# Kernel optimization log

Measured on AMD Instinct MI355X. Metric: run time of the kernel, lower is better.

The kernel has to match this reference:

```python
import jax, jax.numpy as jnp
from jax import lax
import numpy as np

N_BLOCKS = 5; C = 256; K = 1024; NQ = 8; NRES = 4; B = 2; T = 65536


def conv1d(x, w, b, stride=1, padding=0, dilation=1):
    # x: [N,C,T], w: [O,I,k]
    y = lax.conv_general_dilated(x, w, (stride,), [(padding, padding)],
                                 rhs_dilation=(dilation,),
                                 dimension_numbers=('NCH', 'OIH', 'NCH'))
    return y + b[None, :, None]


def conv_transpose1d(x, w, b):
    # PyTorch ConvTranspose1d(k=4, s=2, p=1); w: [in, out, 4]
    wk = jnp.swapaxes(jnp.flip(w, -1), 0, 1)  # [out, in, 4]
    y = lax.conv_general_dilated(x, wk, (1,), [(2, 2)], lhs_dilation=(2,),
                                 dimension_numbers=('NCH', 'OIH', 'NCH'))
    return y + b[None, :, None]


def residual_model(x, w0, b0, w1, b1, dil):
    # ReLU -> dilated conv3 -> ReLU -> conv3
    h = conv1d(jax.nn.relu(x), w0, b0, padding=dil, dilation=dil)
    h = conv1d(jax.nn.relu(h), w1, b1, padding=1)
    return h


def encoder(x, d0w, d0b, dw, db, rw, rb):
    for i in range(N_BLOCKS):
        if i == 0:
            x = conv1d(x, d0w, d0b, stride=2, padding=1)
        else:
            x = conv1d(x, dw[i - 1], db[i - 1], stride=2, padding=1)
        for j in range(NRES):
            dil = 3 ** (j + 1)
            # ResidualBlock.forward: x + model(x)
            x = x + residual_model(x, rw[i, j, 0], rb[i, j, 0], rw[i, j, 1], rb[i, j, 1], dil)
    return x


def decoder(x, rw, rb, uw, ub, ulw, ulb):
    for i in range(N_BLOCKS):
        for j in range(NRES):
            dil = 3 ** (j + 1)
            # DecoderBlock: x = x + ResidualBlock(x) = x + (x + model(x))
            x = x + (x + residual_model(x, rw[i, j, 0], rb[i, j, 0], rw[i, j, 1], rb[i, j, 1], dil))
        if i == N_BLOCKS - 1:
            x = conv_transpose1d(x, ulw, ulb)
        else:
            x = conv_transpose1d(x, uw[i], ub[i])
    return x


def rvq(emb, rvq_sum, rvq_usage):
    # emb: [N, C]; eval-mode residual VQ (no EMA update)
    q = jnp.zeros_like(emb)
    commit = jnp.asarray(0.0, emb.dtype)
    codes = []
    for i in range(NQ):
        cb = rvq_sum[i] / jnp.clip(rvq_usage[i], 1e-5, None)[:, None]  # [K, C]
        res = emb - q
        # argmin of squared distance over codebook rows (||res||^2 constant per column)
        scores = jnp.sum(cb * cb, axis=1)[:, None] - 2.0 * (cb @ res.T)  # [K, N]
        c = jnp.argmin(scores, axis=0)
        eq = cb[c]  # [N, C]
        eq_st = res + lax.stop_gradient(eq - res)  # straight-through
        commit = commit + jnp.mean((lax.stop_gradient(eq_st) - res) ** 2)
        q = q + eq_st
        codes.append(c.astype(jnp.int32))
    return jnp.stack(codes, axis=1), q, commit


def setup_inputs() -> dict:
    key = jax.random.key(0)
    ks = iter(jax.random.split(key, 16))

    def W(shape, fan_in):
        return (jax.random.normal(next(ks), shape, jnp.float32) / np.float32(np.sqrt(fan_in)))

    return {
        'x': jax.random.normal(next(ks), (B, 1, T), jnp.float32),
        'enc_down0_w': W((C, 1, 4), 4),
        'enc_down0_b': jnp.zeros((C,), jnp.float32),
        'enc_down_w': W((N_BLOCKS - 1, C, C, 4), C * 4),
        'enc_down_b': jnp.zeros((N_BLOCKS - 1, C), jnp.float32),
        'enc_res_w': W((N_BLOCKS, NRES, 2, C, C, 3), C * 3),
        'enc_res_b': jnp.zeros((N_BLOCKS, NRES, 2, C), jnp.float32),
        'dec_res_w': W((N_BLOCKS, NRES, 2, C, C, 3), C * 3),
        'dec_res_b': jnp.zeros((N_BLOCKS, NRES, 2, C), jnp.float32),
        'dec_up_w': W((N_BLOCKS - 1, C, C, 4), C * 4),
        'dec_up_b': jnp.zeros((N_BLOCKS - 1, C), jnp.float32),
        'dec_up_last_w': W((C, 1, 4), C * 4),
        'dec_up_last_b': jnp.zeros((1,), jnp.float32),
        'rvq_sum': jax.random.normal(next(ks), (NQ, K, C), jnp.float32) * 0.1,
        'rvq_usage': jnp.ones((NQ, K), jnp.float32),
    }


def reference(x, enc_down0_w, enc_down0_b, enc_down_w, enc_down_b, enc_res_w, enc_res_b,
              dec_res_w, dec_res_b, dec_up_w, dec_up_b, dec_up_last_w, dec_up_last_b,
              rvq_sum, rvq_usage):
    z = encoder(x, enc_down0_w, enc_down0_b, enc_down_w, enc_down_b, enc_res_w, enc_res_b)
    Bz, Cz, Tz = z.shape
    emb = jnp.transpose(z, (0, 2, 1)).reshape(Bz * Tz, Cz)  # (b t) c
    codes, q, commit = rvq(emb, rvq_sum, rvq_usage)
    zq = jnp.transpose(q.reshape(Bz, Tz, Cz), (0, 2, 1))  # b c t
    recon = decoder(zq, dec_res_w, dec_res_b, dec_up_w, dec_up_b, dec_up_last_w, dec_up_last_b)
    return recon, codes, commit
```

## Files before the change

kernel.cpp:

```cpp
#include <hip/hip_runtime.h>
#include <cstdint>

#define DEVFN static __device__ __forceinline__
typedef unsigned short ushort_t;
typedef unsigned int uint_t;
typedef short short8 __attribute__((ext_vector_type(8)));
typedef float f32x4 __attribute__((ext_vector_type(4)));

DEVFN float bf2f(ushort_t h) { return __uint_as_float(((uint_t)h) << 16); }
DEVFN ushort_t bfhi(float f) {
    uint_t u = __float_as_uint(f);
    u += 0x7fffu + ((u >> 16) & 1u);
    return (ushort_t)(u >> 16);
}
DEVFN void fsplit(float f, ushort_t& h, ushort_t& l) {
    h = bfhi(f);
    l = bfhi(f - bf2f(h));
}
DEVFN void relu_pair(uint_t& h, uint_t& l) {
    float f0 = bf2f((ushort_t)(h & 0xffffu)) + bf2f((ushort_t)(l & 0xffffu));
    float f1 = bf2f((ushort_t)(h >> 16)) + bf2f((ushort_t)(l >> 16));
    if (f0 <= 0.f) { h &= 0xffff0000u; l &= 0xffff0000u; }
    if (f1 <= 0.f) { h &= 0x0000ffffu; l &= 0x0000ffffu; }
}

__global__ __launch_bounds__(256)
void wprep3_k(const float* __restrict__ erw, const float* __restrict__ drw,
              ushort_t* __restrict__ wH, ushort_t* __restrict__ wL)
{
    const int gid = blockIdx.x * 256 + threadIdx.x;
    const int conv = gid >> 16;
    const int rem  = gid & 65535;
    const int co = rem >> 8, ci = rem & 255;
    const float* src = (conv < 40) ? (erw + (size_t)conv * 196608)
                                   : (drw + (size_t)(conv - 40) * 196608);
    const float* p = src + ((size_t)co * 256 + ci) * 3;
    ushort_t* oh = wH + (size_t)conv * 196608 + rem;
    ushort_t* ol = wL + (size_t)conv * 196608 + rem;
#pragma unroll
    for (int k = 0; k < 3; ++k) {
        ushort_t h, l; fsplit(p[k], h, l);
        oh[k * 65536] = h; ol[k * 65536] = l;
    }
}

__global__ __launch_bounds__(256)
void wprep4_k(const float* __restrict__ edw, const float* __restrict__ duw,
              ushort_t* __restrict__ wH, ushort_t* __restrict__ wL)
{
    const int gid = blockIdx.x * 256 + threadIdx.x;
    const int conv = gid >> 16;
    const int rem  = gid & 65535;
    const int co = rem >> 8, ci = rem & 255;
    ushort_t* oh = wH + (size_t)conv * 262144 + rem;
    ushort_t* ol = wL + (size_t)conv * 262144 + rem;
#pragma unroll
    for (int k = 0; k < 4; ++k) {
        float f;
        if (conv < 4)  f = edw[(size_t)conv * 262144 + ((size_t)co * 256 + ci) * 4 + k];
        else           f = duw[(size_t)(conv - 4) * 262144 + ((size_t)ci * 256 + co) * 4 + k];
        ushort_t h, l; fsplit(f, h, l);
        oh[k * 65536] = h; ol[k * 65536] = l;
    }
}

template<int TAPS, int STRIDE, bool RELU, int NT, int DMAX>
__global__ __launch_bounds__(256, (NT >= 8) ? 2 : 3)
void convs_k(const ushort_t* __restrict__ inH, const ushort_t* __restrict__ inL,
             const ushort_t* __restrict__ wH, const ushort_t* __restrict__ wL,
             const float* __restrict__ bias,
             const ushort_t* __restrict__ srcH, const ushort_t* __restrict__ srcL,
             float alpha,
             ushort_t* __restrict__ outH, ushort_t* __restrict__ outL,
             int Lin, int Lout, int dil, int pad)
{
    constexpr int ROWS = NT * 16;
    constexpr int SMAX = STRIDE * (ROWS - 1) + (TAPS - 1) * DMAX + 1;
    constexpr int XSB  = SMAX * 40 * 2;
    constexpr int ARENA = (2 * XSB > 16640) ? 2 * XSB : 16640;
    __shared__ __align__(16) char sarena[ARENA];
    ushort_t (*xsH)[40] = (ushort_t(*)[40])(sarena);
    ushort_t (*xsL)[40] = (ushort_t(*)[40])(sarena + XSB);

    const int tid = threadIdx.x;
    const int b = blockIdx.z;
    const int t0 = blockIdx.x * ROWS;
    const int wave = tid >> 6, lane = tid & 63;
    const int quad = lane >> 4, lr = lane & 15;
    const int cow = wave * 64;
    const size_t inbase = (size_t)b * Lin * 256;
    const int S = STRIDE * (ROWS - 1) + (TAPS - 1) * dil + 1;
    const int g0 = STRIDE * t0 - pad;

    f32x4 acc[4][NT];
#pragma unroll
    for (int m = 0; m < 4; ++m)
#pragma unroll
        for (int n = 0; n < NT; ++n) acc[m][n] = (f32x4)0.f;

    for (int chunk = 0; chunk < 8; ++chunk) {
        const int ci0 = chunk * 32;
        __syncthreads();
        for (int idx = tid; idx < S * 4; idx += 256) {
            const int s = idx >> 2, p = idx & 3;
            const int t = g0 + s;
            uint4 hv = make_uint4(0, 0, 0, 0), lv = hv;
            if (t >= 0 && t < Lin) {
                const size_t g = inbase + (size_t)t * 256 + ci0 + p * 8;
                hv = *(const uint4*)(inH + g);
                lv = *(const uint4*)(inL + g);
                if (RELU) {
                    relu_pair(hv.x, lv.x); relu_pair(hv.y, lv.y);
                    relu_pair(hv.z, lv.z); relu_pair(hv.w, lv.w);
                }
            }
            *(uint4*)&xsH[s][p * 8] = hv;
            *(uint4*)&xsL[s][p * 8] = lv;
        }
        __syncthreads();
#pragma unroll
        for (int tap = 0; tap < TAPS; ++tap) {
            const ushort_t* wHt = wH + (size_t)tap * 65536 + ci0 + quad * 8;
            const ushort_t* wLt = wL + (size_t)tap * 65536 + ci0 + quad * 8;
            short8 aH[4], aL[4];
#pragma unroll
            for (int m = 0; m < 4; ++m) {
                const int co = cow + m * 16 + lr;
                aH[m] = *(const short8*)(wHt + co * 256);
                aL[m] = *(const short8*)(wLt + co * 256);
            }
            const int rb = tap * dil;
#pragma unroll
            for (int n = 0; n < NT; ++n) {
                const int srow = STRIDE * (n * 16 + lr) + rb;
                const short8 bH = *(const short8*)&xsH[srow][quad * 8];
                const short8 bL = *(const short8*)&xsL[srow][quad * 8];
#pragma unroll
                for (int m = 0; m < 4; ++m)
                    acc[m][n] = __builtin_amdgcn_mfma_f32_16x16x32_bf16(aH[m], bH, acc[m][n], 0, 0, 0);
#pragma unroll
                for (int m = 0; m < 4; ++m)
                    acc[m][n] = __builtin_amdgcn_mfma_f32_16x16x32_bf16(aH[m], bL, acc[m][n], 0, 0, 0);
#pragma unroll
                for (int m = 0; m < 4; ++m)
                    acc[m][n] = __builtin_amdgcn_mfma_f32_16x16x32_bf16(aL[m], bH, acc[m][n], 0, 0, 0);
            }
        }
    }
    float4 bvv[4];
#pragma unroll
    for (int m = 0; m < 4; ++m)
        bvv[m] = *(const float4*)&bias[cow + m * 16 + quad * 4];
    __syncthreads();
    float (*ebuf)[260] = (float(*)[260])sarena;
#pragma unroll
    for (int n = 0; n < NT; ++n) {
#pragma unroll
        for (int m = 0; m < 4; ++m) {
            float4 v;
            v.x = acc[m][n][0] + bvv[m].x;
            v.y = acc[m][n][1] + bvv[m].y;
            v.z = acc[m][n][2] + bvv[m].z;
            v.w = acc[m][n][3] + bvv[m].w;
            *(float4*)&ebuf[lr][cow + m * 16 + quad * 4] = v;
        }
        __syncthreads();
        {
            const int row = tid >> 4;
            const int c00 = (tid & 15) * 4;
            const int t = t0 + n * 16 + row;
            const size_t gr = ((size_t)b * Lout + t) * 256;
#pragma unroll
            for (int rep = 0; rep < 4; ++rep) {
                const int col = c00 + rep * 64;
                float4 v = *(const float4*)&ebuf[row][col];
                if (alpha != 0.f) {
                    const ushort4 sh = *(const ushort4*)(srcH + gr + col);
                    const ushort4 sl = *(const ushort4*)(srcL + gr + col);
                    v.x += alpha * (bf2f(sh.x) + bf2f(sl.x));
                    v.y += alpha * (bf2f(sh.y) + bf2f(sl.y));
                    v.z += alpha * (bf2f(sh.z) + bf2f(sl.z));
                    v.w += alpha * (bf2f(sh.w) + bf2f(sl.w));
                }
                ushort4 oh, ol;
                fsplit(v.x, oh.x, ol.x); fsplit(v.y, oh.y, ol.y);
                fsplit(v.z, oh.z, ol.z); fsplit(v.w, oh.w, ol.w);
                *(ushort4*)(outH + gr + col) = oh;
                *(ushort4*)(outL + gr + col) = ol;
            }
        }
        __syncthreads();
    }
}

template<int NTc>
__global__ __launch_bounds__(256, 2)
void convt_k(const ushort_t* __restrict__ inH, const ushort_t* __restrict__ inL,
             const ushort_t* __restrict__ wH, const ushort_t* __restrict__ wL,
             const float* __restrict__ bias,
             ushort_t* __restrict__ outH, ushort_t* __restrict__ outL, int Lin)
{
    constexpr int ROWS = NTc * 16;
    constexpr int S = ROWS + 2;
    constexpr int XSB = S * 40 * 2;
    constexpr int ARENA = (2 * XSB > 33280) ? 2 * XSB : 33280;
    __shared__ __align__(16) char sarena[ARENA];
    ushort_t (*xsH)[40] = (ushort_t(*)[40])(sarena);
    ushort_t (*xsL)[40] = (ushort_t(*)[40])(sarena + XSB);

    const int tid = threadIdx.x;
    const int b = blockIdx.z;
    const int m0 = blockIdx.x * ROWS;
    const int Lout = Lin * 2;
    const int wave = tid >> 6, lane = tid & 63;
    const int quad = lane >> 4, lr = lane & 15;
    const int cow = wave * 64;
    const size_t inbase = (size_t)b * Lin * 256;

    f32x4 acc[4][NTc][2];
#pragma unroll
    for (int m = 0; m < 4; ++m)
#pragma unroll
        for (int n = 0; n < NTc; ++n) { acc[m][n][0] = (f32x4)0.f; acc[m][n][1] = (f32x4)0.f; }

    for (int chunk = 0; chunk < 8; ++chunk) {
        const int ci0 = chunk * 32;
        __syncthreads();
        for (int idx = tid; idx < S * 4; idx += 256) {
            const int s = idx >> 2, p = idx & 3;
            const int t = m0 - 1 + s;
            uint4 hv = make_uint4(0, 0, 0, 0), lv = hv;
            if (t >= 0 && t < Lin) {
                const size_t g = inbase + (size_t)t * 256 + ci0 + p * 8;
                hv = *(const uint4*)(inH + g);
                lv = *(const uint4*)(inL + g);
            }
            *(uint4*)&xsH[s][p * 8] = hv;
            *(uint4*)&xsL[s][p * 8] = lv;
        }
        __syncthreads();
#pragma unroll
        for (int tap = 0; tap < 4; ++tap) {
            const int ph = (tap == 0 || tap == 2) ? 1 : 0;
            const int sh = (tap == 0) ? 1 : ((tap == 3) ? -1 : 0);
            const ushort_t* wHt = wH + (size_t)tap * 65536 + ci0 + quad * 8;
            const ushort_t* wLt = wL + (size_t)tap * 65536 + ci0 + quad * 8;
            short8 aH[4], aL[4];
#pragma unroll
            for (int m = 0; m < 4; ++m) {
                const int co = cow + m * 16 + lr;
                aH[m] = *(const short8*)(wHt + co * 256);
                aL[m] = *(const short8*)(wLt + co * 256);
            }
#pragma unroll
            for (int n = 0; n < NTc; ++n) {
                const int srow = n * 16 + lr + sh + 1;
                const short8 bH = *(const short8*)&xsH[srow][quad * 8];
                const short8 bL = *(const short8*)&xsL[srow][quad * 8];
#pragma unroll
                for (int m = 0; m < 4; ++m)
                    acc[m][n][ph] = __builtin_amdgcn_mfma_f32_16x16x32_bf16(aH[m], bH, acc[m][n][ph], 0, 0, 0);
#pragma unroll
                for (int m = 0; m < 4; ++m)
                    acc[m][n][ph] = __builtin_amdgcn_mfma_f32_16x16x32_bf16(aH[m], bL, acc[m][n][ph], 0, 0, 0);
#pragma unroll
                for (int m = 0; m < 4; ++m)
                    acc[m][n][ph] = __builtin_amdgcn_mfma_f32_16x16x32_bf16(aL[m], bH, acc[m][n][ph], 0, 0, 0);
            }
        }
    }
    float4 bvv[4];
#pragma unroll
    for (int m = 0; m < 4; ++m)
        bvv[m] = *(const float4*)&bias[cow + m * 16 + quad * 4];
    __syncthreads();
    float (*ebuf)[260] = (float(*)[260])sarena;
#pragma unroll
    for (int n = 0; n < NTc; ++n) {
#pragma unroll
        for (int m = 0; m < 4; ++m) {
#pragma unroll
            for (int ph = 0; ph < 2; ++ph) {
                float4 v;
                v.x = acc[m][n][ph][0] + bvv[m].x;
                v.y = acc[m][n][ph][1] + bvv[m].y;
                v.z = acc[m][n][ph][2] + bvv[m].z;
                v.w = acc[m][n][ph][3] + bvv[m].w;
                *(float4*)&ebuf[2 * lr + ph][cow + m * 16 + quad * 4] = v;
            }
        }
        __syncthreads();
        {
            const int baset = 2 * (m0 + n * 16);
#pragma unroll
            for (int h = 0; h < 8; ++h) {
                const int row = (tid >> 4) + 16 * (h >> 2);
                const int col = (tid & 15) * 4 + (h & 3) * 64;
                const int t = baset + row;
                const size_t gr = ((size_t)b * Lout + t) * 256 + col;
                float4 v = *(const float4*)&ebuf[row][col];
                ushort4 oh, ol;
                fsplit(v.x, oh.x, ol.x); fsplit(v.y, oh.y, ol.y);
                fsplit(v.z, oh.z, ol.z); fsplit(v.w, oh.w, ol.w);
                *(ushort4*)(outH + gr) = oh;
                *(ushort4*)(outL + gr) = ol;
            }
        }
        __syncthreads();
    }
}

__global__ __launch_bounds__(256)
void down0_k2(const float* __restrict__ x, const float* __restrict__ w,
              const float* __restrict__ bias,
              ushort_t* __restrict__ outH, ushort_t* __restrict__ outL)
{
    const int t = blockIdx.x;
    const int b = blockIdx.y;
    const int co = threadIdx.x;
    const float* xb = x + (size_t)b * 65536;
    const float4 wv = *(const float4*)(w + co * 4);
    float s = bias[co];
    const int ti0 = 2 * t - 1;
    if (ti0 >= 0)      s = fmaf(xb[ti0], wv.x, s);
    s = fmaf(xb[ti0 + 1], wv.y, s);
    s = fmaf(xb[ti0 + 2], wv.z, s);
    if (ti0 + 3 < 65536) s = fmaf(xb[ti0 + 3], wv.w, s);
    ushort_t h, l; fsplit(s, h, l);
    const size_t g = ((size_t)b * 32768 + t) * 256 + co;
    outH[g] = h; outL[g] = l;
}

__global__ __launch_bounds__(256)
void uplast_k2(const ushort_t* __restrict__ inH, const ushort_t* __restrict__ inL,
               const float* __restrict__ w, const float* __restrict__ bias,
               float* __restrict__ out, int Lin)
{
    const int m = blockIdx.x * 256 + threadIdx.x;
    const int b = blockIdx.y;
    const float bv = bias[0];
    float aE = bv, aO = bv;
    const size_t base = (size_t)b * Lin * 256;
    const ushort_t* r0H = inH + base + (size_t)m * 256;
    const ushort_t* r0L = inL + base + (size_t)m * 256;
    const bool hasM = (m > 0), hasP = (m + 1 < Lin);
    for (int c0 = 0; c0 < 256; c0 += 8) {
        uint4 h0 = *(const uint4*)(r0H + c0);
        uint4 l0 = *(const uint4*)(r0L + c0);
        uint4 hm = make_uint4(0,0,0,0), lm = hm, hp = hm, lp = hm;
        if (hasM) { hm = *(const uint4*)(r0H - 256 + c0); lm = *(const uint4*)(r0L - 256 + c0); }
        if (hasP) { hp = *(const uint4*)(r0H + 256 + c0); lp = *(const uint4*)(r0L + 256 + c0); }
        const uint_t* h0p = (const uint_t*)&h0; const uint_t* l0p = (const uint_t*)&l0;
        const uint_t* hmp = (const uint_t*)&hm; const uint_t* lmp = (const uint_t*)&lm;
        const uint_t* hpp = (const uint_t*)&hp; const uint_t* lpp = (const uint_t*)&lp;
#pragma unroll
        for (int e = 0; e < 4; ++e) {
#pragma unroll
            for (int half = 0; half < 2; ++half) {
                const int sh = half * 16;
                const int ci = c0 + e * 2 + half;
                const float x0  = bf2f((ushort_t)(h0p[e] >> sh)) + bf2f((ushort_t)(l0p[e] >> sh));
                const float xm1 = bf2f((ushort_t)(hmp[e] >> sh)) + bf2f((ushort_t)(lmp[e] >> sh));
                const float xp1 = bf2f((ushort_t)(hpp[e] >> sh)) + bf2f((ushort_t)(lpp[e] >> sh));
                const float4 wv = *(const float4*)(w + ci * 4);
                aE = fmaf(x0, wv.y, fmaf(xm1, wv.w, aE));
                aO = fmaf(xp1, wv.x, fmaf(x0, wv.z, aO));
            }
        }
    }
    *(float2*)(out + (size_t)b * 2 * Lin + 2 * m) = make_float2(aE, aO);
}

__global__ void emb_k(const ushort_t* __restrict__ H, const ushort_t* __restrict__ L,
                      float* __restrict__ emb)
{
    const size_t g = (size_t)blockIdx.x * 256 + threadIdx.x;
    emb[g] = bf2f(H[g]) + bf2f(L[g]);
}
__global__ void qsplit_k(const float* __restrict__ q,
                         ushort_t* __restrict__ H, ushort_t* __restrict__ L)
{
    const size_t g = (size_t)blockIdx.x * 256 + threadIdx.x;
    ushort_t h, l; fsplit(q[g], h, l);
    H[g] = h; L[g] = l;
}

__global__ __launch_bounds__(256)
void rvq_cb_k(const float* __restrict__ sum, const float* __restrict__ usage,
              float* __restrict__ cb, float* __restrict__ cbT,
              float* __restrict__ cbn, int iq)
{
    const int k = blockIdx.x, c = threadIdx.x;
    const float den = fmaxf(usage[iq * 1024 + k], 1e-5f);
    const float v = sum[((size_t)iq * 1024 + k) * 256 + c] / den;
    cb[(size_t)k * 256 + c] = v;
    cbT[(size_t)c * 1024 + k] = v;
    float s = v * v;
    for (int off = 32; off; off >>= 1) s += __shfl_down(s, off, 64);
    __shared__ float ls[4];
    if ((c & 63) == 0) ls[c >> 6] = s;
    __syncthreads();
    if (c == 0) cbn[k] = ls[0] + ls[1] + ls[2] + ls[3];
}

DEVFN unsigned int ordbits(float f)
{
    unsigned u = __float_as_uint(f);
    return (u & 0x80000000u) ? ~u : (u | 0x80000000u);
}
DEVFN unsigned long long shfl_xor_u64(unsigned long long v, int mask)
{
    int lo = (int)(v & 0xffffffffull), hi = (int)(v >> 32);
    lo = __shfl_xor(lo, mask, 64);
    hi = __shfl_xor(hi, mask, 64);
    return ((unsigned long long)(unsigned)hi << 32) | (unsigned)lo;
}

__global__ __launch_bounds__(256)
void rvq_argmin_k(const float* __restrict__ emb, const float* __restrict__ q,
                  const float* __restrict__ cbT, const float* __restrict__ cbn,
                  int* __restrict__ codes, float* __restrict__ codes_out, int iq)
{
    const int n0 = blockIdx.x * 16;
    const int tid = threadIdx.x;
    __shared__ float res[16][256];
    for (int idx = tid; idx < 16 * 256; idx += 256) {
        int nl = idx >> 8, c = idx & 255;
        size_t g = (size_t)(n0 + nl) * 256 + c;
        res[nl][c] = emb[g] - q[g];
    }
    __syncthreads();
    float dot[16][4];
#pragma unroll
    for (int nl = 0; nl < 16; ++nl)
#pragma unroll
        for (int j = 0; j < 4; ++j) dot[nl][j] = 0.f;

    const float* cbtp = cbT + tid * 4;
    for (int c = 0; c < 256; ++c) {
        const float4 cbv = *(const float4*)(cbtp + (size_t)c * 1024);
#pragma unroll
        for (int nl = 0; nl < 16; ++nl) {
            const float r = res[nl][c];
            dot[nl][0] = fmaf(cbv.x, r, dot[nl][0]);
            dot[nl][1] = fmaf(cbv.y, r, dot[nl][1]);
            dot[nl][2] = fmaf(cbv.z, r, dot[nl][2]);
            dot[nl][3] = fmaf(cbv.w, r, dot[nl][3]);
        }
    }
    const float4 nrm = *(const float4*)(cbn + tid * 4);
    __shared__ unsigned long long wred[4][16];
    const int wave = tid >> 6, lane = tid & 63;
#pragma unroll
    for (int nl = 0; nl < 16; ++nl) {
        float s0 = nrm.x - 2.f * dot[nl][0];
        float s1 = nrm.y - 2.f * dot[nl][1];
        float s2 = nrm.z - 2.f * dot[nl][2];
        float s3 = nrm.w - 2.f * dot[nl][3];
        unsigned long long key =
            ((unsigned long long)ordbits(s0) << 32) | (unsigned)(tid * 4 + 0);
        unsigned long long k1 =
            ((unsigned long long)ordbits(s1) << 32) | (unsigned)(tid * 4 + 1);
        unsigned long long k2 =
            ((unsigned long long)ordbits(s2) << 32) | (unsigned)(tid * 4 + 2);
        unsigned long long k3 =
            ((unsigned long long)ordbits(s3) << 32) | (unsigned)(tid * 4 + 3);
        if (k1 < key) key = k1;
        if (k2 < key) key = k2;
        if (k3 < key) key = k3;
        for (int off = 32; off; off >>= 1) {
            unsigned long long o = shfl_xor_u64(key, off);
            if (o < key) key = o;
        }
        if (lane == 0) wred[wave][nl] = key;
    }
    __syncthreads();
    if (tid < 16) {
        unsigned long long bkey = wred[0][tid];
        if (wred[1][tid] < bkey) bkey = wred[1][tid];
        if (wred[2][tid] < bkey) bkey = wred[2][tid];
        if (wred[3][tid] < bkey) bkey = wred[3][tid];
        const int code = (int)(bkey & 0xffffffffull);
        codes[(size_t)(n0 + tid) * 8 + iq] = code;
        codes_out[(size_t)(n0 + tid) * 8 + iq] = (float)code;
    }
}

__global__ __launch_bounds__(256)
void rvq_update_k(const float* __restrict__ emb, float* __restrict__ q,
                  const float* __restrict__ cb, const int* __restrict__ codes,
                  float* __restrict__ commit, int iq)
{
    const int n = blockIdx.x, c = threadIdx.x;
    const int code = codes[(size_t)n * 8 + iq];
    const size_t g = (size_t)n * 256 + c;
    const float qv = q[g] + cb[(size_t)code * 256 + c];
    q[g] = qv;
    const float e = qv - emb[g];
    float s = e * e;
    for (int off = 32; off; off >>= 1) s += __shfl_down(s, off, 64);
    __shared__ float ls[4];
    if ((c & 63) == 0) ls[c >> 6] = s;
    __syncthreads();
    if (c == 0) atomicAdd(commit, ls[0] + ls[1] + ls[2] + ls[3]);
}

__global__ void commit_write_k(const float* __restrict__ commit, float* __restrict__ out)
{
    out[0] = commit[0] * (1.f / (4096.f * 256.f));
}

extern "C" void kernel_launch(void* const* d_in, const int* in_sizes, int n_in,
                              void* d_out, int out_size, void* d_ws, size_t ws_size,
                              hipStream_t stream)
{
    const float* x    = (const float*)d_in[0];
    const float* ed0w = (const float*)d_in[1];
    const float* ed0b = (const float*)d_in[2];
    const float* edw  = (const float*)d_in[3];
    const float* edb  = (const float*)d_in[4];
    const float* erw  = (const float*)d_in[5];
    const float* erb  = (const float*)d_in[6];
    const float* drw  = (const float*)d_in[7];
    const float* drb  = (const float*)d_in[8];
    const float* duw  = (const float*)d_in[9];
    const float* dub  = (const float*)d_in[10];
    const float* dulw = (const float*)d_in[11];
    const float* dulb = (const float*)d_in[12];
    const float* rsum = (const float*)d_in[13];
    const float* rusg = (const float*)d_in[14];
    float* out = (float*)d_out;

    char* base = (char*)d_ws;
    size_t o = 0;
    ushort_t* wH3 = (ushort_t*)(base + o); o += 31457280;
    ushort_t* wL3 = (ushort_t*)(base + o); o += 31457280;
    ushort_t* w4H = (ushort_t*)(base + o); o += 4194304;
    ushort_t* w4L = (ushort_t*)(base + o); o += 4194304;
    ushort_t* AH  = (ushort_t*)(base + o); o += 33554432;
    ushort_t* AL  = (ushort_t*)(base + o); o += 33554432;
    ushort_t* BH  = (ushort_t*)(base + o); o += 33554432;
    ushort_t* BL  = (ushort_t*)(base + o); o += 33554432;
    float* emb    = (float*)(base + o);    o += 4194304;
    float* q      = (float*)(base + o);    o += 4194304;
    float* commit = (float*)(base + o);    o += 64;
    float* cb     = (float*)(base + o);    o += 1048576;
    float* cbT    = (float*)(base + o);    o += 1048576;
    float* cbn    = (float*)(base + o);    o += 4096;
    int*   codes  = (int*)(base + o);      o += 131072;

    static const int DIL[4] = {3, 9, 27, 81};

    hipMemsetAsync(q, 0, 4194304 + 64, stream);

    wprep3_k<<<20480, 256, 0, stream>>>(erw, drw, wH3, wL3);
    wprep4_k<<<2048, 256, 0, stream>>>(edw, duw, w4H, w4L);

    auto conv3 = [&](const ushort_t* iH, const ushort_t* iL,
                     const ushort_t* wh, const ushort_t* wl, const float* bb,
                     const ushort_t* sH, const ushort_t* sL, float alpha,
                     ushort_t* oH, ushort_t* oL, int L, int d) {
        if (L >= 16384)
            convs_k<3, 1, true, 8, 81><<<dim3(L / 128, 1, 2), 256, 0, stream>>>(
                iH, iL, wh, wl, bb, sH, sL, alpha, oH, oL, L, L, d, d);
        else if (L >= 8192)
            convs_k<3, 1, true, 4, 81><<<dim3(L / 64, 1, 2), 256, 0, stream>>>(
                iH, iL, wh, wl, bb, sH, sL, alpha, oH, oL, L, L, d, d);
        else if (L >= 4096)
            convs_k<3, 1, true, 2, 81><<<dim3(L / 32, 1, 2), 256, 0, stream>>>(
                iH, iL, wh, wl, bb, sH, sL, alpha, oH, oL, L, L, d, d);
        else
            convs_k<3, 1, true, 1, 81><<<dim3(L / 16, 1, 2), 256, 0, stream>>>(
                iH, iL, wh, wl, bb, sH, sL, alpha, oH, oL, L, L, d, d);
    };

    down0_k2<<<dim3(32768, 2), 256, 0, stream>>>(x, ed0w, ed0b, AH, AL);
    int L = 32768;
    for (int i = 0; i < 5; ++i) {
        if (i > 0) {
            const ushort_t* wh = w4H + (size_t)(i - 1) * 262144;
            const ushort_t* wl = w4L + (size_t)(i - 1) * 262144;
            const int Lout = L / 2;
            if (Lout >= 16384)
                convs_k<4, 2, false, 8, 1><<<dim3(Lout / 128, 1, 2), 256, 0, stream>>>(
                    AH, AL, wh, wl, edb + (i - 1) * 256, AH, AL, 0.f, BH, BL, L, Lout, 1, 1);
            else if (Lout >= 8192)
                convs_k<4, 2, false, 4, 1><<<dim3(Lout / 64, 1, 2), 256, 0, stream>>>(
                    AH, AL, wh, wl, edb + (i - 1) * 256, AH, AL, 0.f, BH, BL, L, Lout, 1, 1);
            else if (Lout >= 4096)
                convs_k<4, 2, false, 2, 1><<<dim3(Lout / 32, 1, 2), 256, 0, stream>>>(
                    AH, AL, wh, wl, edb + (i - 1) * 256, AH, AL, 0.f, BH, BL, L, Lout, 1, 1);
            else
                convs_k<4, 2, false, 1, 1><<<dim3(Lout / 16, 1, 2), 256, 0, stream>>>(
                    AH, AL, wh, wl, edb + (i - 1) * 256, AH, AL, 0.f, BH, BL, L, Lout, 1, 1);
            ushort_t* t;
            t = AH; AH = BH; BH = t;
            t = AL; AL = BL; BL = t;
            L = Lout;
        }
        for (int j = 0; j < 4; ++j) {
            const int d = DIL[j];
            const size_t u = (size_t)(i * 4 + j) * 2;
            conv3(AH, AL, wH3 + (u + 0) * 196608, wL3 + (u + 0) * 196608,
                  erb + (u + 0) * 256, AH, AL, 0.f, BH, BL, L, d);
            conv3(BH, BL, wH3 + (u + 1) * 196608, wL3 + (u + 1) * 196608,
                  erb + (u + 1) * 256, AH, AL, 1.f, AH, AL, L, 1);
        }
    }

    emb_k<<<4096, 256, 0, stream>>>(AH, AL, emb);
    for (int iq = 0; iq < 8; ++iq) {
        rvq_cb_k<<<1024, 256, 0, stream>>>(rsum, rusg, cb, cbT, cbn, iq);
        rvq_argmin_k<<<256, 256, 0, stream>>>(emb, q, cbT, cbn, codes, out + 131072, iq);
        rvq_update_k<<<4096, 256, 0, stream>>>(emb, q, cb, codes, commit, iq);
    }
    qsplit_k<<<4096, 256, 0, stream>>>(q, AH, AL);

    L = 2048;
    for (int i = 0; i < 5; ++i) {
        for (int j = 0; j < 4; ++j) {
            const int d = DIL[j];
            const size_t u = 40 + (size_t)(i * 4 + j) * 2;
            conv3(AH, AL, wH3 + (u + 0) * 196608, wL3 + (u + 0) * 196608,
                  drb + ((size_t)(i * 4 + j) * 2 + 0) * 256, AH, AL, 0.f, BH, BL, L, d);
            conv3(BH, BL, wH3 + (u + 1) * 196608, wL3 + (u + 1) * 196608,
                  drb + ((size_t)(i * 4 + j) * 2 + 1) * 256, AH, AL, 2.f, AH, AL, L, 1);
        }
        if (i < 4) {
            const ushort_t* wh = w4H + (size_t)(4 + i) * 262144;
            const ushort_t* wl = w4L + (size_t)(4 + i) * 262144;
            if (L >= 16384)
                convt_k<4><<<dim3(L / 64, 1, 2), 256, 0, stream>>>(
                    AH, AL, wh, wl, dub + i * 256, BH, BL, L);
            else if (L >= 8192)
                convt_k<4><<<dim3(L / 64, 1, 2), 256, 0, stream>>>(
                    AH, AL, wh, wl, dub + i * 256, BH, BL, L);
            else if (L >= 4096)
                convt_k<2><<<dim3(L / 32, 1, 2), 256, 0, stream>>>(
                    AH, AL, wh, wl, dub + i * 256, BH, BL, L);
            else
                convt_k<1><<<dim3(L / 16, 1, 2), 256, 0, stream>>>(
                    AH, AL, wh, wl, dub + i * 256, BH, BL, L);
            ushort_t* t;
            t = AH; AH = BH; BH = t;
            t = AL; AL = BL; BL = t;
            L *= 2;
        } else {
            uplast_k2<<<dim3(L / 256, 2), 256, 0, stream>>>(AH, AL, dulw, dulb, out, L);
        }
    }

    commit_write_k<<<1, 1, 0, stream>>>(commit, out + 163840);
}
```

Baseline: 6.102 ms.

## Split conv3 output channels across blocks and specialize strided downsample kernel

```diff
diff --git a/kernel.cpp b/kernel.cpp
--- a/kernel.cpp
+++ b/kernel.cpp
@@ -64,39 +64,41 @@
     }
 }
 
-template<int TAPS, int STRIDE, bool RELU, int NT, int DMAX>
-__global__ __launch_bounds__(256, (NT >= 8) ? 2 : 3)
-void convs_k(const ushort_t* __restrict__ inH, const ushort_t* __restrict__ inL,
-             const ushort_t* __restrict__ wH, const ushort_t* __restrict__ wL,
-             const float* __restrict__ bias,
-             const ushort_t* __restrict__ srcH, const ushort_t* __restrict__ srcL,
-             float alpha,
-             ushort_t* __restrict__ outH, ushort_t* __restrict__ outL,
-             int Lin, int Lout, int dil, int pad)
-{
-    constexpr int ROWS = NT * 16;
-    constexpr int SMAX = STRIDE * (ROWS - 1) + (TAPS - 1) * DMAX + 1;
+template<bool RELU, int NTT>
+__global__ __launch_bounds__(256, 4)
+void conv3n_k(const ushort_t* __restrict__ inH, const ushort_t* __restrict__ inL,
+              const ushort_t* __restrict__ wH, const ushort_t* __restrict__ wL,
+              const float* __restrict__ bias,
+              const ushort_t* __restrict__ srcH, const ushort_t* __restrict__ srcL,
+              float alpha,
+              ushort_t* __restrict__ outH, ushort_t* __restrict__ outL,
+              int L, int dil)
+{
+    constexpr int ROWS = NTT * 16;
+    constexpr int SMAX = ROWS + 162;
     constexpr int XSB  = SMAX * 40 * 2;
-    constexpr int ARENA = (2 * XSB > 16640) ? 2 * XSB : 16640;
+    constexpr int EBUF = 16 * 132 * 4;
+    constexpr int ARENA = (2 * XSB > EBUF) ? 2 * XSB : EBUF;
     __shared__ __align__(16) char sarena[ARENA];
     ushort_t (*xsH)[40] = (ushort_t(*)[40])(sarena);
     ushort_t (*xsL)[40] = (ushort_t(*)[40])(sarena + XSB);
 
     const int tid = threadIdx.x;
     const int b = blockIdx.z;
+    const int co0 = blockIdx.y * 128;
     const int t0 = blockIdx.x * ROWS;
     const int wave = tid >> 6, lane = tid & 63;
     const int quad = lane >> 4, lr = lane & 15;
-    const int cow = wave * 64;
-    const size_t inbase = (size_t)b * Lin * 256;
-    const int S = STRIDE * (ROWS - 1) + (TAPS - 1) * dil + 1;
-    const int g0 = STRIDE * t0 - pad;
-
-    f32x4 acc[4][NT];
-#pragma unroll
-    for (int m = 0; m < 4; ++m)
-#pragma unroll
-        for (int n = 0; n < NT; ++n) acc[m][n] = (f32x4)0.f;
+    const int cow = co0 + wave * 32;
+    const size_t inbase = (size_t)b * L * 256;
+    const int S = ROWS + 2 * dil;
+    const int g0 = t0 - dil;
+
+    f32x4 acc[2][NTT];
+#pragma unroll
+    for (int m = 0; m < 2; ++m)
+#pragma unroll
+        for (int n = 0; n < NTT; ++n) acc[m][n] = (f32x4)0.f;
 
     for (int chunk = 0; chunk < 8; ++chunk) {
         const int ci0 = chunk * 32;
@@ -105,7 +107,7 @@
             const int s = idx >> 2, p = idx & 3;
             const int t = g0 + s;
             uint4 hv = make_uint4(0, 0, 0, 0), lv = hv;
-            if (t >= 0 && t < Lin) {
+            if (t >= 0 && t < L) {
                 const size_t g = inbase + (size_t)t * 256 + ci0 + p * 8;
                 hv = *(const uint4*)(inH + g);
                 lv = *(const uint4*)(inL + g);
@@ -119,59 +121,59 @@
         }
         __syncthreads();
 #pragma unroll
-        for (int tap = 0; tap < TAPS; ++tap) {
+        for (int tap = 0; tap < 3; ++tap) {
             const ushort_t* wHt = wH + (size_t)tap * 65536 + ci0 + quad * 8;
             const ushort_t* wLt = wL + (size_t)tap * 65536 + ci0 + quad * 8;
-            short8 aH[4], aL[4];
-#pragma unroll
-            for (int m = 0; m < 4; ++m) {
+            short8 aH[2], aL[2];
+#pragma unroll
+            for (int m = 0; m < 2; ++m) {
                 const int co = cow + m * 16 + lr;
                 aH[m] = *(const short8*)(wHt + co * 256);
                 aL[m] = *(const short8*)(wLt + co * 256);
             }
             const int rb = tap * dil;
 #pragma unroll
-            for (int n = 0; n < NT; ++n) {
-                const int srow = STRIDE * (n * 16 + lr) + rb;
+            for (int n = 0; n < NTT; ++n) {
+                const int srow = n * 16 + lr + rb;
                 const short8 bH = *(const short8*)&xsH[srow][quad * 8];
                 const short8 bL = *(const short8*)&xsL[srow][quad * 8];
 #pragma unroll
-                for (int m = 0; m < 4; ++m)
+                for (int m = 0; m < 2; ++m)
                     acc[m][n] = __builtin_amdgcn_mfma_f32_16x16x32_bf16(aH[m], bH, acc[m][n], 0, 0, 0);
 #pragma unroll
-                for (int m = 0; m < 4; ++m)
+                for (int m = 0; m < 2; ++m)
                     acc[m][n] = __builtin_amdgcn_mfma_f32_16x16x32_bf16(aH[m], bL, acc[m][n], 0, 0, 0);
 #pragma unroll
-                for (int m = 0; m < 4; ++m)
+                for (int m = 0; m < 2; ++m)
                     acc[m][n] = __builtin_amdgcn_mfma_f32_16x16x32_bf16(aL[m], bH, acc[m][n], 0, 0, 0);
             }
         }
     }
-    float4 bvv[4];
-#pragma unroll
-    for (int m = 0; m < 4; ++m)
+    float4 bvv[2];
+#pragma unroll
+    for (int m = 0; m < 2; ++m)
         bvv[m] = *(const float4*)&bias[cow + m * 16 + quad * 4];
     __syncthreads();
-    float (*ebuf)[260] = (float(*)[260])sarena;
-#pragma unroll
-    for (int n = 0; n < NT; ++n) {
-#pragma unroll
-        for (int m = 0; m < 4; ++m) {
+    float (*ebuf)[132] = (float(*)[132])sarena;
+#pragma unroll
+    for (int n = 0; n < NTT; ++n) {
+#pragma unroll
+        for (int m = 0; m < 2; ++m) {
             float4 v;
             v.x = acc[m][n][0] + bvv[m].x;
             v.y = acc[m][n][1] + bvv[m].y;
             v.z = acc[m][n][2] + bvv[m].z;
             v.w = acc[m][n][3] + bvv[m].w;
-            *(float4*)&ebuf[lr][cow + m * 16 + quad * 4] = v;
+            *(float4*)&ebuf[lr][wave * 32 + m * 16 + quad * 4] = v;
         }
         __syncthreads();
         {
             const int row = tid >> 4;
             const int c00 = (tid & 15) * 4;
             const int t = t0 + n * 16 + row;
-            const size_t gr = ((size_t)b * Lout + t) * 256;
-#pragma unroll
-            for (int rep = 0; rep < 4; ++rep) {
+            const size_t gr = ((size_t)b * L + t) * 256 + co0;
+#pragma unroll
+            for (int rep = 0; rep < 2; ++rep) {
                 const int col = c00 + rep * 64;
                 float4 v = *(const float4*)&ebuf[row][col];
                 if (alpha != 0.f) {
@@ -182,6 +184,120 @@
                     v.z += alpha * (bf2f(sh.z) + bf2f(sl.z));
                     v.w += alpha * (bf2f(sh.w) + bf2f(sl.w));
                 }
+                ushort4 oh, ol;
+                fsplit(v.x, oh.x, ol.x); fsplit(v.y, oh.y, ol.y);
+                fsplit(v.z, oh.z, ol.z); fsplit(v.w, oh.w, ol.w);
+                *(ushort4*)(outH + gr + col) = oh;
+                *(ushort4*)(outL + gr + col) = ol;
+            }
+        }
+        __syncthreads();
+    }
+}
+
+template<int NT>
+__global__ __launch_bounds__(256, (NT >= 8) ? 2 : 3)
+void convs_k(const ushort_t* __restrict__ inH, const ushort_t* __restrict__ inL,
+             const ushort_t* __restrict__ wH, const ushort_t* __restrict__ wL,
+             const float* __restrict__ bias,
+             ushort_t* __restrict__ outH, ushort_t* __restrict__ outL,
+             int Lin, int Lout)
+{
+    constexpr int ROWS = NT * 16;
+    constexpr int SMAX = 2 * (ROWS - 1) + 4;
+    constexpr int XSB  = SMAX * 40 * 2;
+    constexpr int ARENA = (2 * XSB > 16640) ? 2 * XSB : 16640;
+    __shared__ __align__(16) char sarena[ARENA];
+    ushort_t (*xsH)[40] = (ushort_t(*)[40])(sarena);
+    ushort_t (*xsL)[40] = (ushort_t(*)[40])(sarena + XSB);
+
+    const int tid = threadIdx.x;
+    const int b = blockIdx.z;
+    const int t0 = blockIdx.x * ROWS;
+    const int wave = tid >> 6, lane = tid & 63;
+    const int quad = lane >> 4, lr = lane & 15;
+    const int cow = wave * 64;
+    const size_t inbase = (size_t)b * Lin * 256;
+    const int S = 2 * (ROWS - 1) + 4;
+    const int g0 = 2 * t0 - 1;
+
+    f32x4 acc[4][NT];
+#pragma unroll
+    for (int m = 0; m < 4; ++m)
+#pragma unroll
+        for (int n = 0; n < NT; ++n) acc[m][n] = (f32x4)0.f;
+
+    for (int chunk = 0; chunk < 8; ++chunk) {
+        const int ci0 = chunk * 32;
+        __syncthreads();
+        for (int idx = tid; idx < S * 4; idx += 256) {
+            const int s = idx >> 2, p = idx & 3;
+            const int t = g0 + s;
+            uint4 hv = make_uint4(0, 0, 0, 0), lv = hv;
+            if (t >= 0 && t < Lin) {
+                const size_t g = inbase + (size_t)t * 256 + ci0 + p * 8;
+                hv = *(const uint4*)(inH + g);
+                lv = *(const uint4*)(inL + g);
+            }
+            *(uint4*)&xsH[s][p * 8] = hv;
+            *(uint4*)&xsL[s][p * 8] = lv;
+        }
+        __syncthreads();
+#pragma unroll
+        for (int tap = 0; tap < 4; ++tap) {
+            const ushort_t* wHt = wH + (size_t)tap * 65536 + ci0 + quad * 8;
+            const ushort_t* wLt = wL + (size_t)tap * 65536 + ci0 + quad * 8;
+            short8 aH[4], aL[4];
+#pragma unroll
+            for (int m = 0; m < 4; ++m) {
+                const int co = cow + m * 16 + lr;
+                aH[m] = *(const short8*)(wHt + co * 256);
+                aL[m] = *(const short8*)(wLt + co * 256);
+            }
+#pragma unroll
+            for (int n = 0; n < NT; ++n) {
+                const int srow = 2 * (n * 16 + lr) + tap;
+                const short8 bH = *(const short8*)&xsH[srow][quad * 8];
+                const short8 bL = *(const short8*)&xsL[srow][quad * 8];
+#pragma unroll
+                for (int m = 0; m < 4; ++m)
+                    acc[m][n] = __builtin_amdgcn_mfma_f32_16x16x32_bf16(aH[m], bH, acc[m][n], 0, 0, 0);
+#pragma unroll
+                for (int m = 0; m < 4; ++m)
+                    acc[m][n] = __builtin_amdgcn_mfma_f32_16x16x32_bf16(aH[m], bL, acc[m][n], 0, 0, 0);
+#pragma unroll
+                for (int m = 0; m < 4; ++m)
+                    acc[m][n] = __builtin_amdgcn_mfma_f32_16x16x32_bf16(aL[m], bH, acc[m][n], 0, 0, 0);
+            }
+        }
+    }
+    float4 bvv[4];
+#pragma unroll
+    for (int m = 0; m < 4; ++m)
+        bvv[m] = *(const float4*)&bias[cow + m * 16 + quad * 4];
+    __syncthreads();
+    float (*ebuf)[260] = (float(*)[260])sarena;
+#pragma unroll
+    for (int n = 0; n < NT; ++n) {
+#pragma unroll
+        for (int m = 0; m < 4; ++m) {
+            float4 v;
+            v.x = acc[m][n][0] + bvv[m].x;
+            v.y = acc[m][n][1] + bvv[m].y;
+            v.z = acc[m][n][2] + bvv[m].z;
+            v.w = acc[m][n][3] + bvv[m].w;
+            *(float4*)&ebuf[lr][cow + m * 16 + quad * 4] = v;
+        }
+        __syncthreads();
+        {
+            const int row = tid >> 4;
+            const int c00 = (tid & 15) * 4;
+            const int t = t0 + n * 16 + row;
+            const size_t gr = ((size_t)b * Lout + t) * 256;
+#pragma unroll
+            for (int rep = 0; rep < 4; ++rep) {
+                const int col = c00 + rep * 64;
+                float4 v = *(const float4*)&ebuf[row][col];
                 ushort4 oh, ol;
                 fsplit(v.x, oh.x, ol.x); fsplit(v.y, oh.y, ol.y);
                 fsplit(v.z, oh.z, ol.z); fsplit(v.w, oh.w, ol.w);
@@ -561,17 +677,11 @@
                      const ushort_t* sH, const ushort_t* sL, float alpha,
                      ushort_t* oH, ushort_t* oL, int L, int d) {
         if (L >= 16384)
-            convs_k<3, 1, true, 8, 81><<<dim3(L / 128, 1, 2), 256, 0, stream>>>(
-                iH, iL, wh, wl, bb, sH, sL, alpha, oH, oL, L, L, d, d);
-        else if (L >= 8192)
-            convs_k<3, 1, true, 4, 81><<<dim3(L / 64, 1, 2), 256, 0, stream>>>(
-                iH, iL, wh, wl, bb, sH, sL, alpha, oH, oL, L, L, d, d);
-        else if (L >= 4096)
-            convs_k<3, 1, true, 2, 81><<<dim3(L / 32, 1, 2), 256, 0, stream>>>(
-                iH, iL, wh, wl, bb, sH, sL, alpha, oH, oL, L, L, d, d);
+            conv3n_k<true, 4><<<dim3(L / 64, 2, 2), 256, 0, stream>>>(
+                iH, iL, wh, wl, bb, sH, sL, alpha, oH, oL, L, d);
         else
-            convs_k<3, 1, true, 1, 81><<<dim3(L / 16, 1, 2), 256, 0, stream>>>(
-                iH, iL, wh, wl, bb, sH, sL, alpha, oH, oL, L, L, d, d);
+            conv3n_k<true, 2><<<dim3(L / 32, 2, 2), 256, 0, stream>>>(
+                iH, iL, wh, wl, bb, sH, sL, alpha, oH, oL, L, d);
     };
 
     down0_k2<<<dim3(32768, 2), 256, 0, stream>>>(x, ed0w, ed0b, AH, AL);
@@ -582,17 +692,14 @@
             const ushort_t* wl = w4L + (size_t)(i - 1) * 262144;
             const int Lout = L / 2;
             if (Lout >= 16384)
-                convs_k<4, 2, false, 8, 1><<<dim3(Lout / 128, 1, 2), 256, 0, stream>>>(
-                    AH, AL, wh, wl, edb + (i - 1) * 256, AH, AL, 0.f, BH, BL, L, Lout, 1, 1);
-            else if (Lout >= 8192)
-                convs_k<4, 2, false, 4, 1><<<dim3(Lout / 64, 1, 2), 256, 0, stream>>>(
-                    AH, AL, wh, wl, edb + (i - 1) * 256, AH, AL, 0.f, BH, BL, L, Lout, 1, 1);
+                convs_k<8><<<dim3(Lout / 128, 1, 2), 256, 0, stream>>>(
+                    AH, AL, wh, wl, edb + (i - 1) * 256, BH, BL, L, Lout);
             else if (Lout >= 4096)
-                convs_k<4, 2, false, 2, 1><<<dim3(Lout / 32, 1, 2), 256, 0, stream>>>(
-                    AH, AL, wh, wl, edb + (i - 1) * 256, AH, AL, 0.f, BH, BL, L, Lout, 1, 1);
+                convs_k<4><<<dim3(Lout / 64, 1, 2), 256, 0, stream>>>(
+                    AH, AL, wh, wl, edb + (i - 1) * 256, BH, BL, L, Lout);
             else
-                convs_k<4, 2, false, 1, 1><<<dim3(Lout / 16, 1, 2), 256, 0, stream>>>(
-                    AH, AL, wh, wl, edb + (i - 1) * 256, AH, AL, 0.f, BH, BL, L, Lout, 1, 1);
+                convs_k<2><<<dim3(Lout / 32, 1, 2), 256, 0, stream>>>(
+                    AH, AL, wh, wl, edb + (i - 1) * 256, BH, BL, L, Lout);
             ushort_t* t;
             t = AH; AH = BH; BH = t;
             t = AL; AL = BL; BL = t;
@@ -629,10 +736,7 @@
         if (i < 4) {
             const ushort_t* wh = w4H + (size_t)(4 + i) * 262144;
             const ushort_t* wl = w4L + (size_t)(4 + i) * 262144;
-            if (L >= 16384)
-                convt_k<4><<<dim3(L / 64, 1, 2), 256, 0, stream>>>(
-                    AH, AL, wh, wl, dub + i * 256, BH, BL, L);
-            else if (L >= 8192)
+            if (L >= 8192)
                 convt_k<4><<<dim3(L / 64, 1, 2), 256, 0, stream>>>(
                     AH, AL, wh, wl, dub + i * 256, BH, BL, L);
             else if (L >= 4096)
```

Result: slower. 6.363 ms (+4.3%).
